# Kernel tuning notes

Hardware: AMD Instinct MI355X
Metric: run time of the kernel (lower is better)

Reference implementation:

```python
import jax, jax.numpy as jnp
import numpy as np

B, T, D, H = 32, 1024, 768, 768

def setup_inputs() -> dict:
    key = jax.random.key(0)
    k0, k1, k2, k3 = jax.random.split(key, 4)
    inputs = jax.random.normal(k0, (B, T, D), dtype=jnp.float32)
    # packed-sequence lengths: sorted descending, in [1, T]
    lengths = jnp.sort(jax.random.randint(k1, (B,), 1, T + 1))[::-1]
    # parameters (orthogonal-block init approximated by scaled gaussian)
    W_in = jax.random.normal(k2, (6 * H, D), dtype=jnp.float32) / np.sqrt(D)
    b_in = jnp.zeros((6 * H,), dtype=jnp.float32)
    W_s = jax.random.normal(k3, (5 * H, H), dtype=jnp.float32) / np.sqrt(H)
    # state bias: forget-gate block initialized to 1.0, rest 0
    b_s = jnp.zeros((5 * H,), dtype=jnp.float32).at[H:2 * H].set(1.0)
    return {"inputs": inputs, "W_in": W_in, "b_in": b_in,
            "W_s": W_s, "b_s": b_s, "lengths": lengths}

def reference(inputs, W_in, b_in, W_s, b_s, lengths):
    Bb, Tt, Dd = inputs.shape
    Hh = W_s.shape[1]
    # precompute all input projections in one big GEMM: [B,T,6H]
    proj_in = jnp.einsum('btd,kd->btk', inputs, W_in) + b_in
    mask = jnp.arange(Tt)[None, :] < lengths[:, None]  # [B,T] valid timesteps

    def step(carry, xs):
        h, c = carry                    # [B,H] each
        pi, m = xs                      # pi: [B,6H], m: [B] bool
        ps = h @ W_s.T + b_s            # [B,5H] recurrent GEMM
        i = jax.nn.sigmoid(pi[:, 0*Hh:1*Hh] + ps[:, 0*Hh:1*Hh])
        f = jax.nn.sigmoid(pi[:, 1*Hh:2*Hh] + ps[:, 1*Hh:2*Hh])
        g = jnp.tanh(pi[:, 2*Hh:3*Hh] + ps[:, 2*Hh:3*Hh])
        o = jax.nn.sigmoid(pi[:, 3*Hh:4*Hh] + ps[:, 3*Hh:4*Hh])
        c_new = i * g + f * c
        out = o * jnp.tanh(c_new)
        # highway mix
        hw = jax.nn.sigmoid(pi[:, 4*Hh:5*Hh] + ps[:, 4*Hh:5*Hh])
        out = hw * out + (1.0 - hw) * pi[:, 5*Hh:6*Hh]
        mcol = m[:, None]
        h_next = jnp.where(mcol, out, h)      # freeze state past seq length
        c_next = jnp.where(mcol, c_new, c)
        y = jnp.where(mcol, out, 0.0)          # zero outputs past length
        return (h_next, c_next), y

    h0 = jnp.zeros((Bb, Hh), dtype=inputs.dtype)
    c0 = jnp.zeros((Bb, Hh), dtype=inputs.dtype)
    pi_t = jnp.swapaxes(proj_in, 0, 1)  # [T,B,6H]
    m_t = jnp.swapaxes(mask, 0, 1)      # [T,B]
    (h_fin, c_fin), ys = jax.lax.scan(step, (h0, c0), (pi_t, m_t))
    return jnp.swapaxes(ys, 0, 1)       # [B,T,H]
```

## Files before the change

### kernel.cpp

```cpp
#include <hip/hip_runtime.h>
#include <hip/hip_bf16.h>

#define Bb 32
#define Tt 1024
#define Dd 768
#define Hh 768
#define NGRP 2
#define BPG 96
#define GB  16
#define CPB 8
#define NTHREADS 192

#define NWELE ((size_t)6 * Hh * Dd)
#define NSELE ((size_t)5 * Hh * Hh)
#define WS_FLAGS 4096
#define WS_HB    8192
#define HBSZ     (GB * Hh * 2)
#define WS_WGT   (WS_HB + 4 * HBSZ)
#define WS_NEED  (WS_WGT + (NWELE + NSELE) * 2)

typedef short short8 __attribute__((ext_vector_type(8)));
typedef float f4 __attribute__((ext_vector_type(4)));

__device__ __forceinline__ float bf2f(ushort u) {
    unsigned x = (unsigned)u << 16;
    return __builtin_bit_cast(float, x);
}
__device__ __forceinline__ ushort f2bf(float f) {
    unsigned u = __builtin_bit_cast(unsigned, f);
    return (ushort)((u + 0x7fffu + ((u >> 16) & 1u)) >> 16);
}
__device__ __forceinline__ float sigm(float x) { return 1.0f / (1.0f + __expf(-x)); }
__device__ __forceinline__ float tanh_(float x) {
    float e = __expf(2.0f * x);
    return 1.0f - 2.0f / (e + 1.0f);
}

__global__ void prep_nb(const int* __restrict__ len, int* __restrict__ nbArr) {
    int t = blockIdx.x * 256 + threadIdx.x;
    if (t < Tt) {
        int c = 0;
#pragma unroll
        for (int b = 0; b < Bb; ++b) c += (len[b] > t) ? 1 : 0;
        nbArr[t] = c;
    }
}

__global__ void conv_w(const void* __restrict__ Win, const void* __restrict__ Ws,
                       const void* __restrict__ bs, ushort* __restrict__ wOut) {
    const bool isbf = (((const unsigned*)bs)[384] != 0u);
    size_t i = ((size_t)blockIdx.x * 256 + threadIdx.x) * 8;
    if (i >= NWELE + NSELE) return;
    const void* src = (i < NWELE) ? Win : Ws;
    size_t off = (i < NWELE) ? i : (i - NWELE);
    if (isbf) {
        *(uint4*)(wOut + i) = *(const uint4*)((const ushort*)src + off);
    } else {
        const f4* s = (const f4*)((const float*)src + off);
        f4 a = s[0], c = s[1];
        uint4 v;
        v.x = (unsigned)f2bf(a[0]) | ((unsigned)f2bf(a[1]) << 16);
        v.y = (unsigned)f2bf(a[2]) | ((unsigned)f2bf(a[3]) << 16);
        v.z = (unsigned)f2bf(c[0]) | ((unsigned)f2bf(c[1]) << 16);
        v.w = (unsigned)f2bf(c[2]) | ((unsigned)f2bf(c[3]) << 16);
        *(uint4*)(wOut + i) = v;
    }
}

__global__ __launch_bounds__(NTHREADS, 1) void lstm_main(
    const void* __restrict__ inp, const void* __restrict__ bin,
    const void* __restrict__ bs, const int* __restrict__ len,
    void* __restrict__ y, const int* __restrict__ nbArr,
    unsigned* flags, ushort* hbAll, const ushort* __restrict__ wbf)
{
    __shared__ ushort wsL[48 * 776];
    __shared__ ushort hA[GB * 776];
    __shared__ float accT[3][16][16];

    const bool isbf = (((const unsigned*)bs)[384] != 0u);

    const int tid  = threadIdx.x;
    const int lane = tid & 63;
    const int wave = tid >> 6;
    const int g    = blockIdx.x & 1;
    const int w    = blockIdx.x >> 1;
    const int n0   = w * CPB;

    for (int i = tid; i < 48 * 776 / 8; i += NTHREADS)
        *(uint4*)&wsL[i * 8] = uint4{0u, 0u, 0u, 0u};
    const ushort* wbfS = wbf + NWELE;
    __syncthreads();
    for (int i = tid; i < 40 * 96; i += NTHREADS) {
        int c = i / 96, ch = i - c * 96;
        *(uint4*)&wsL[c * 776 + ch * 8] =
            *(const uint4*)(wbfS + ((size_t)((c >> 3) * Hh + n0 + (c & 7))) * Hh + ch * 8);
    }

    float B0 = 0, B1 = 0, B2 = 0, B3 = 0, B4 = 0, B5 = 0, cReg = 0.0f;
    int lenb = 0;
    if (tid < 128) {
        int j = tid & 7, n = n0 + j;
        if (isbf) {
            const ushort* bi = (const ushort*)bin; const ushort* bsp = (const ushort*)bs;
            B0 = bf2f(bi[0 * Hh + n]) + bf2f(bsp[0 * Hh + n]);
            B1 = bf2f(bi[1 * Hh + n]) + bf2f(bsp[1 * Hh + n]);
            B2 = bf2f(bi[2 * Hh + n]) + bf2f(bsp[2 * Hh + n]);
            B3 = bf2f(bi[3 * Hh + n]) + bf2f(bsp[3 * Hh + n]);
            B4 = bf2f(bi[4 * Hh + n]) + bf2f(bsp[4 * Hh + n]);
            B5 = bf2f(bi[5 * Hh + n]);
        } else {
            const float* bi = (const float*)bin; const float* bsp = (const float*)bs;
            B0 = bi[0 * Hh + n] + bsp[0 * Hh + n];
            B1 = bi[1 * Hh + n] + bsp[1 * Hh + n];
            B2 = bi[2 * Hh + n] + bsp[2 * Hh + n];
            B3 = bi[3 * Hh + n] + bsp[3 * Hh + n];
            B4 = bi[4 * Hh + n] + bsp[4 * Hh + n];
            B5 = bi[5 * Hh + n];
        }
        lenb = len[g * GB + (tid >> 3)];
    }

    const int kq = (lane >> 4) << 3;
    const ushort* aP = &hA[(lane & 15) * 776 + kq];
    const int aoff = ((lane >> 4) * 32) + ((lane & 15) * 2);
    const int cc = wave * 16 + (lane & 15);
    const uint4* bPx = (const uint4*)(wbf + ((size_t)((cc >> 3) * Hh + n0 + (cc & 7))) * Dd + kq);
    const ushort* wsP = &wsL[cc * 776 + kq];

    unsigned* flg = flags + g * 128;
    ushort* hb[2] = {hbAll + (g * 2 + 0) * (HBSZ / 2),
                     hbAll + (g * 2 + 1) * (HBSZ / 2)};
    int p = 0;
    long gmax = (1L << 22);
    __syncthreads();

    int tDone = Tt;
    for (int t = 0; t < Tt; ++t) {
        int nbg = nbArr[t] - g * GB;
        nbg = nbg < 0 ? 0 : (nbg > GB ? GB : nbg);
        if (nbg == 0) { tDone = t; break; }

        if (isbf) {
            const ushort* xi = (const ushort*)inp;
            for (int i = tid; i < GB * 96; i += NTHREADS) {
                int row = i / 96, c8 = i - row * 96;
                *(uint4*)&hA[row * 776 + c8 * 8] =
                    *((const uint4*)(xi + ((size_t)(g * GB + row) * Tt + t) * Dd) + c8);
            }
        } else {
            const float* xf = (const float*)inp;
            for (int i = tid; i < GB * 96; i += NTHREADS) {
                int row = i / 96, c8 = i - row * 96;
                const f4* s = (const f4*)(xf + ((size_t)(g * GB + row) * Tt + t) * Dd + c8 * 8);
                f4 a = s[0], c = s[1];
                uint4 v;
                v.x = (unsigned)f2bf(a[0]) | ((unsigned)f2bf(a[1]) << 16);
                v.y = (unsigned)f2bf(a[2]) | ((unsigned)f2bf(a[3]) << 16);
                v.z = (unsigned)f2bf(c[0]) | ((unsigned)f2bf(c[1]) << 16);
                v.w = (unsigned)f2bf(c[2]) | ((unsigned)f2bf(c[3]) << 16);
                *(uint4*)&hA[row * 776 + c8 * 8] = v;
            }
        }
        __syncthreads();

        f4 acc0 = {0, 0, 0, 0}, acc1 = {0, 0, 0, 0};
#pragma unroll
        for (int kb = 0; kb < 24; ++kb) {
            short8 a = __builtin_bit_cast(short8, *(const uint4*)(aP + kb * 32));
            short8 b = __builtin_bit_cast(short8, bPx[kb * 4]);
            if (kb & 1) acc1 = __builtin_amdgcn_mfma_f32_16x16x32_bf16(a, b, acc1, 0, 0, 0);
            else        acc0 = __builtin_amdgcn_mfma_f32_16x16x32_bf16(a, b, acc0, 0, 0, 0);
        }

        if (t > 0) {
            const unsigned target = (unsigned)t;
            long guard = 0;
            for (;;) {
                unsigned f0 = __hip_atomic_load(flg + lane, __ATOMIC_RELAXED,
                                                __HIP_MEMORY_SCOPE_AGENT);
                unsigned f1 = __hip_atomic_load(flg + 32 + lane, __ATOMIC_RELAXED,
                                                __HIP_MEMORY_SCOPE_AGENT);
                bool ok = (f0 >= target) && (f1 >= target);
                if (__all(ok)) break;
                if (++guard > gmax) break;
                __builtin_amdgcn_s_sleep(1);
            }
        }
        __asm__ volatile("" ::: "memory");

        {
            const unsigned long long* aB = (const unsigned long long*)hb[p];
#pragma unroll
            for (int kb = 0; kb < 24; ++kb) {
                unsigned long long v0 = __hip_atomic_load(aB + kb * 128 + aoff,
                                                          __ATOMIC_RELAXED,
                                                          __HIP_MEMORY_SCOPE_AGENT);
                unsigned long long v1 = __hip_atomic_load(aB + kb * 128 + aoff + 1,
                                                          __ATOMIC_RELAXED,
                                                          __HIP_MEMORY_SCOPE_AGENT);
                short8 a;
                __builtin_memcpy(&a, &v0, 8);
                __builtin_memcpy((char*)&a + 8, &v1, 8);
                short8 b = __builtin_bit_cast(short8, *(const uint4*)(wsP + kb * 32));
                if (kb & 1) acc1 = __builtin_amdgcn_mfma_f32_16x16x32_bf16(a, b, acc1, 0, 0, 0);
                else        acc0 = __builtin_amdgcn_mfma_f32_16x16x32_bf16(a, b, acc0, 0, 0, 0);
            }
        }
        {
            f4 s = acc0 + acc1;
            int r0 = (lane >> 4) * 4, col = lane & 15;
#pragma unroll
            for (int i = 0; i < 4; ++i) accT[wave][r0 + i][col] = s[i];
        }
        __syncthreads();

        float outv = 0.0f; bool act = false;
        if (tid < 128) {
            int b = tid >> 3, j = tid & 7;
            float v0 = accT[(0 * 8 + j) >> 4][b][(0 * 8 + j) & 15];
            float v1 = accT[(1 * 8 + j) >> 4][b][(1 * 8 + j) & 15];
            float v2 = accT[(2 * 8 + j) >> 4][b][(2 * 8 + j) & 15];
            float v3 = accT[(3 * 8 + j) >> 4][b][(3 * 8 + j) & 15];
            float v4 = accT[(4 * 8 + j) >> 4][b][(4 * 8 + j) & 15];
            float v5 = accT[(5 * 8 + j) >> 4][b][(5 * 8 + j) & 15];
            float ii = sigm(v0 + B0);
            float ff = sigm(v1 + B1);
            float gg = tanh_(v2 + B2);
            float oo = sigm(v3 + B3);
            float hw = sigm(v4 + B4);
            float p5 = v5 + B5;
            float cn = ii * gg + ff * cReg;
            outv = oo * tanh_(cn);
            outv = hw * outv + (1.0f - hw) * p5;
            act = t < lenb;
            if (act) cReg = cn;

            unsigned myv = (unsigned)f2bf(outv);
            int lane6 = tid & 63;
            int g0 = lane6 & ~3;
            unsigned a0 = (unsigned)__shfl((int)myv, g0 + 0);
            unsigned a1 = (unsigned)__shfl((int)myv, g0 + 1);
            unsigned a2 = (unsigned)__shfl((int)myv, g0 + 2);
            unsigned a3 = (unsigned)__shfl((int)myv, g0 + 3);
            if ((lane6 & 3) == 0 && act) {
                unsigned long long vv = (unsigned long long)(a0 & 0xffffu)
                    | ((unsigned long long)(a1 & 0xffffu) << 16)
                    | ((unsigned long long)(a2 & 0xffffu) << 32)
                    | ((unsigned long long)(a3 & 0xffffu) << 48);
                __hip_atomic_store(
                    (unsigned long long*)(hb[p ^ 1] + w * 128 + b * 8 + j),
                    vv, __ATOMIC_RELAXED, __HIP_MEMORY_SCOPE_AGENT);
            }
        }
        __syncthreads();
        if (tid == 0)
            __hip_atomic_store(flg + w, (unsigned)(t + 1),
                               __ATOMIC_RELAXED, __HIP_MEMORY_SCOPE_AGENT);

        if (tid < 128) {
            int b = tid >> 3, j = tid & 7;
            size_t oi = ((size_t)(g * GB + b) * Tt + t) * Hh + n0 + j;
            if (isbf) ((ushort*)y)[oi] = act ? f2bf(outv) : (ushort)0;
            else      ((float*)y)[oi]  = act ? outv : 0.0f;
        }
        p ^= 1;
    }

    if (tid < 128) {
        int b = tid >> 3, j = tid & 7;
        for (int t = tDone; t < Tt; ++t) {
            size_t oi = ((size_t)(g * GB + b) * Tt + t) * Hh + n0 + j;
            if (isbf) ((ushort*)y)[oi] = 0; else ((float*)y)[oi] = 0.0f;
        }
    }
}

extern "C" void kernel_launch(void* const* d_in, const int* in_sizes, int n_in,
                              void* d_out, int out_size, void* d_ws, size_t ws_size,
                              hipStream_t stream) {
    const void* inp = d_in[0];
    const void* Win = d_in[1];
    const void* bin = d_in[2];
    const void* Ws  = d_in[3];
    const void* bs  = d_in[4];
    const int*  len = (const int*)d_in[5];

    if (ws_size < WS_NEED) return;

    char* ws = (char*)d_ws;
    int* nbArr      = (int*)ws;
    unsigned* flags = (unsigned*)(ws + WS_FLAGS);
    ushort* hbAll   = (ushort*)(ws + WS_HB);
    ushort* wbf     = (ushort*)(ws + WS_WGT);

    hipMemsetAsync(d_ws, 0, WS_WGT, stream);
    prep_nb<<<4, 256, 0, stream>>>(len, nbArr);
    conv_w<<<3168, 256, 0, stream>>>(Win, Ws, bs, wbf);
    lstm_main<<<NGRP * BPG, NTHREADS, 0, stream>>>(inp, bin, bs, len, d_out,
                                                   nbArr, flags, hbAll, wbf);
}
```

Before: 9.403 ms.

## Prefetch next-step inputs, use per-step counters, and batch output stores

The next timestep's input row is prefetched into registers and double-buffered in LDS, so the global load overlaps the current step's GEMM and wait. The per-block flag array polled by all lanes is replaced with one atomic counter per timestep that each wave increments after its h stores. Outputs are staged in LDS and written in groups of 16 timesteps, and four MFMA accumulators replace two. Costs are more registers for the prefetch, more LDS, and a grid-wide counter that every wave hits with an atomic add.

```diff
diff --git a/kernel.cpp b/kernel.cpp
--- a/kernel.cpp
+++ b/kernel.cpp
@@ -10,13 +10,15 @@
 #define GB  16
 #define CPB 8
 #define NTHREADS 192
+#define CNT_TGT (2 * BPG)
 
 #define NWELE ((size_t)6 * Hh * Dd)
 #define NSELE ((size_t)5 * Hh * Hh)
-#define WS_FLAGS 4096
-#define WS_HB    8192
+#define WS_NB    4096
+#define WS_FLG   8192
+#define WS_HBOFF (WS_NB + WS_FLG)
 #define HBSZ     (GB * Hh * 2)
-#define WS_WGT   (WS_HB + 4 * HBSZ)
+#define WS_WGT   (WS_HBOFF + 4 * HBSZ)
 #define WS_NEED  (WS_WGT + (NWELE + NSELE) * 2)
 
 typedef short short8 __attribute__((ext_vector_type(8)));
@@ -74,8 +76,9 @@
     unsigned* flags, ushort* hbAll, const ushort* __restrict__ wbf)
 {
     __shared__ ushort wsL[48 * 776];
-    __shared__ ushort hA[GB * 776];
+    __shared__ ushort hA[2][16 * 776];
     __shared__ float accT[3][16][16];
+    __shared__ float yBuf[16][128];
 
     const bool isbf = (((const unsigned*)bs)[384] != 0u);
 
@@ -121,17 +124,39 @@
     }
 
     const int kq = (lane >> 4) << 3;
-    const ushort* aP = &hA[(lane & 15) * 776 + kq];
+    const int aOff = (lane & 15) * 776 + kq;
     const int aoff = ((lane >> 4) * 32) + ((lane & 15) * 2);
     const int cc = wave * 16 + (lane & 15);
     const uint4* bPx = (const uint4*)(wbf + ((size_t)((cc >> 3) * Hh + n0 + (cc & 7))) * Dd + kq);
     const ushort* wsP = &wsL[cc * 776 + kq];
 
-    unsigned* flg = flags + g * 128;
+    unsigned* cnt = flags + g * Tt;
     ushort* hb[2] = {hbAll + (g * 2 + 0) * (HBSZ / 2),
                      hbAll + (g * 2 + 1) * (HBSZ / 2)};
     int p = 0;
     long gmax = (1L << 22);
+
+    if (isbf) {
+        const ushort* xi = (const ushort*)inp;
+        for (int i = tid; i < GB * 96; i += NTHREADS) {
+            int row = i / 96, c8 = i - row * 96;
+            *(uint4*)&hA[0][row * 776 + c8 * 8] =
+                *((const uint4*)(xi + ((size_t)(g * GB + row) * Tt) * Dd) + c8);
+        }
+    } else {
+        const float* xf = (const float*)inp;
+        for (int i = tid; i < GB * 96; i += NTHREADS) {
+            int row = i / 96, c8 = i - row * 96;
+            const f4* s = (const f4*)(xf + ((size_t)(g * GB + row) * Tt) * Dd + c8 * 8);
+            f4 a = s[0], c = s[1];
+            uint4 v;
+            v.x = (unsigned)f2bf(a[0]) | ((unsigned)f2bf(a[1]) << 16);
+            v.y = (unsigned)f2bf(a[2]) | ((unsigned)f2bf(a[3]) << 16);
+            v.z = (unsigned)f2bf(c[0]) | ((unsigned)f2bf(c[1]) << 16);
+            v.w = (unsigned)f2bf(c[2]) | ((unsigned)f2bf(c[3]) << 16);
+            *(uint4*)&hA[0][row * 776 + c8 * 8] = v;
+        }
+    }
     __syncthreads();
 
     int tDone = Tt;
@@ -140,48 +165,48 @@
         nbg = nbg < 0 ? 0 : (nbg > GB ? GB : nbg);
         if (nbg == 0) { tDone = t; break; }
 
-        if (isbf) {
-            const ushort* xi = (const ushort*)inp;
-            for (int i = tid; i < GB * 96; i += NTHREADS) {
-                int row = i / 96, c8 = i - row * 96;
-                *(uint4*)&hA[row * 776 + c8 * 8] =
-                    *((const uint4*)(xi + ((size_t)(g * GB + row) * Tt + t) * Dd) + c8);
-            }
-        } else {
-            const float* xf = (const float*)inp;
-            for (int i = tid; i < GB * 96; i += NTHREADS) {
-                int row = i / 96, c8 = i - row * 96;
-                const f4* s = (const f4*)(xf + ((size_t)(g * GB + row) * Tt + t) * Dd + c8 * 8);
-                f4 a = s[0], c = s[1];
-                uint4 v;
-                v.x = (unsigned)f2bf(a[0]) | ((unsigned)f2bf(a[1]) << 16);
-                v.y = (unsigned)f2bf(a[2]) | ((unsigned)f2bf(a[3]) << 16);
-                v.z = (unsigned)f2bf(c[0]) | ((unsigned)f2bf(c[1]) << 16);
-                v.w = (unsigned)f2bf(c[2]) | ((unsigned)f2bf(c[3]) << 16);
-                *(uint4*)&hA[row * 776 + c8 * 8] = v;
-            }
-        }
-        __syncthreads();
-
+        uint4 pfA[8], pfB[8];
+        const bool havePf = (t + 1 < Tt);
+        if (havePf) {
+            if (isbf) {
+                const ushort* xi = (const ushort*)inp;
+#pragma unroll
+                for (int ii = 0; ii < 8; ++ii) {
+                    int i = tid + ii * NTHREADS;
+                    int row = i / 96, c8 = i - row * 96;
+                    pfA[ii] = *((const uint4*)(xi + ((size_t)(g * GB + row) * Tt + (t + 1)) * Dd) + c8);
+                }
+            } else {
+                const float* xf = (const float*)inp;
+#pragma unroll
+                for (int ii = 0; ii < 8; ++ii) {
+                    int i = tid + ii * NTHREADS;
+                    int row = i / 96, c8 = i - row * 96;
+                    const uint4* s = (const uint4*)(xf + ((size_t)(g * GB + row) * Tt + (t + 1)) * Dd + c8 * 8);
+                    pfA[ii] = s[0]; pfB[ii] = s[1];
+                }
+            }
+        }
+
+        const ushort* aP = &hA[t & 1][0] + aOff;
         f4 acc0 = {0, 0, 0, 0}, acc1 = {0, 0, 0, 0};
+        f4 acc2 = {0, 0, 0, 0}, acc3 = {0, 0, 0, 0};
 #pragma unroll
         for (int kb = 0; kb < 24; ++kb) {
             short8 a = __builtin_bit_cast(short8, *(const uint4*)(aP + kb * 32));
             short8 b = __builtin_bit_cast(short8, bPx[kb * 4]);
-            if (kb & 1) acc1 = __builtin_amdgcn_mfma_f32_16x16x32_bf16(a, b, acc1, 0, 0, 0);
-            else        acc0 = __builtin_amdgcn_mfma_f32_16x16x32_bf16(a, b, acc0, 0, 0, 0);
+            switch (kb & 3) {
+            case 0: acc0 = __builtin_amdgcn_mfma_f32_16x16x32_bf16(a, b, acc0, 0, 0, 0); break;
+            case 1: acc1 = __builtin_amdgcn_mfma_f32_16x16x32_bf16(a, b, acc1, 0, 0, 0); break;
+            case 2: acc2 = __builtin_amdgcn_mfma_f32_16x16x32_bf16(a, b, acc2, 0, 0, 0); break;
+            default: acc3 = __builtin_amdgcn_mfma_f32_16x16x32_bf16(a, b, acc3, 0, 0, 0); break;
+            }
         }
 
         if (t > 0) {
-            const unsigned target = (unsigned)t;
             long guard = 0;
-            for (;;) {
-                unsigned f0 = __hip_atomic_load(flg + lane, __ATOMIC_RELAXED,
-                                                __HIP_MEMORY_SCOPE_AGENT);
-                unsigned f1 = __hip_atomic_load(flg + 32 + lane, __ATOMIC_RELAXED,
-                                                __HIP_MEMORY_SCOPE_AGENT);
-                bool ok = (f0 >= target) && (f1 >= target);
-                if (__all(ok)) break;
+            while (__hip_atomic_load(cnt + (t - 1), __ATOMIC_RELAXED,
+                                     __HIP_MEMORY_SCOPE_AGENT) < (unsigned)CNT_TGT) {
                 if (++guard > gmax) break;
                 __builtin_amdgcn_s_sleep(1);
             }
@@ -202,19 +227,54 @@
                 __builtin_memcpy(&a, &v0, 8);
                 __builtin_memcpy((char*)&a + 8, &v1, 8);
                 short8 b = __builtin_bit_cast(short8, *(const uint4*)(wsP + kb * 32));
-                if (kb & 1) acc1 = __builtin_amdgcn_mfma_f32_16x16x32_bf16(a, b, acc1, 0, 0, 0);
-                else        acc0 = __builtin_amdgcn_mfma_f32_16x16x32_bf16(a, b, acc0, 0, 0, 0);
+                switch (kb & 3) {
+                case 0: acc0 = __builtin_amdgcn_mfma_f32_16x16x32_bf16(a, b, acc0, 0, 0, 0); break;
+                case 1: acc1 = __builtin_amdgcn_mfma_f32_16x16x32_bf16(a, b, acc1, 0, 0, 0); break;
+                case 2: acc2 = __builtin_amdgcn_mfma_f32_16x16x32_bf16(a, b, acc2, 0, 0, 0); break;
+                default: acc3 = __builtin_amdgcn_mfma_f32_16x16x32_bf16(a, b, acc3, 0, 0, 0); break;
+                }
             }
         }
         {
-            f4 s = acc0 + acc1;
+            f4 s = (acc0 + acc1) + (acc2 + acc3);
             int r0 = (lane >> 4) * 4, col = lane & 15;
 #pragma unroll
             for (int i = 0; i < 4; ++i) accT[wave][r0 + i][col] = s[i];
         }
         __syncthreads();
 
-        float outv = 0.0f; bool act = false;
+        if (havePf) {
+            ushort* hN = &hA[(t + 1) & 1][0];
+            if (isbf) {
+#pragma unroll
+                for (int ii = 0; ii < 8; ++ii) {
+                    int i = tid + ii * NTHREADS;
+                    int row = i / 96, c8 = i - row * 96;
+                    *(uint4*)&hN[row * 776 + c8 * 8] = pfA[ii];
+                }
+            } else {
+#pragma unroll
+                for (int ii = 0; ii < 8; ++ii) {
+                    int i = tid + ii * NTHREADS;
+                    int row = i / 96, c8 = i - row * 96;
+                    float f0 = __builtin_bit_cast(float, pfA[ii].x);
+                    float f1 = __builtin_bit_cast(float, pfA[ii].y);
+                    float f2 = __builtin_bit_cast(float, pfA[ii].z);
+                    float f3 = __builtin_bit_cast(float, pfA[ii].w);
+                    float f4_ = __builtin_bit_cast(float, pfB[ii].x);
+                    float f5 = __builtin_bit_cast(float, pfB[ii].y);
+                    float f6 = __builtin_bit_cast(float, pfB[ii].z);
+                    float f7 = __builtin_bit_cast(float, pfB[ii].w);
+                    uint4 v;
+                    v.x = (unsigned)f2bf(f0) | ((unsigned)f2bf(f1) << 16);
+                    v.y = (unsigned)f2bf(f2) | ((unsigned)f2bf(f3) << 16);
+                    v.z = (unsigned)f2bf(f4_) | ((unsigned)f2bf(f5) << 16);
+                    v.w = (unsigned)f2bf(f6) | ((unsigned)f2bf(f7) << 16);
+                    *(uint4*)&hN[row * 776 + c8 * 8] = v;
+                }
+            }
+        }
+
         if (tid < 128) {
             int b = tid >> 3, j = tid & 7;
             float v0 = accT[(0 * 8 + j) >> 4][b][(0 * 8 + j) & 15];
@@ -230,10 +290,11 @@
             float hw = sigm(v4 + B4);
             float p5 = v5 + B5;
             float cn = ii * gg + ff * cReg;
-            outv = oo * tanh_(cn);
+            float outv = oo * tanh_(cn);
             outv = hw * outv + (1.0f - hw) * p5;
-            act = t < lenb;
+            bool act = t < lenb;
             if (act) cReg = cn;
+            yBuf[t & 15][tid] = act ? outv : 0.0f;
 
             unsigned myv = (unsigned)f2bf(outv);
             int lane6 = tid & 63;
@@ -251,23 +312,36 @@
                     (unsigned long long*)(hb[p ^ 1] + w * 128 + b * 8 + j),
                     vv, __ATOMIC_RELAXED, __HIP_MEMORY_SCOPE_AGENT);
             }
+            __asm__ volatile("s_waitcnt vmcnt(0)" ::: "memory");
+            if ((tid & 63) == 0)
+                __hip_atomic_fetch_add(cnt + t, 1u, __ATOMIC_RELAXED,
+                                       __HIP_MEMORY_SCOPE_AGENT);
         }
         __syncthreads();
-        if (tid == 0)
-            __hip_atomic_store(flg + w, (unsigned)(t + 1),
-                               __ATOMIC_RELAXED, __HIP_MEMORY_SCOPE_AGENT);
-
-        if (tid < 128) {
+
+        if ((t & 15) == 15 && tid < 128) {
             int b = tid >> 3, j = tid & 7;
-            size_t oi = ((size_t)(g * GB + b) * Tt + t) * Hh + n0 + j;
-            if (isbf) ((ushort*)y)[oi] = act ? f2bf(outv) : (ushort)0;
-            else      ((float*)y)[oi]  = act ? outv : 0.0f;
+            int tBase = t - 15;
+#pragma unroll
+            for (int r = 0; r < 16; ++r) {
+                size_t oi = ((size_t)(g * GB + b) * Tt + (tBase + r)) * Hh + n0 + j;
+                float yv = yBuf[r][tid];
+                if (isbf) ((ushort*)y)[oi] = f2bf(yv);
+                else      ((float*)y)[oi]  = yv;
+            }
         }
         p ^= 1;
     }
 
     if (tid < 128) {
         int b = tid >> 3, j = tid & 7;
+        int tBase = tDone & ~15;
+        for (int r = 0; r < (tDone & 15); ++r) {
+            size_t oi = ((size_t)(g * GB + b) * Tt + (tBase + r)) * Hh + n0 + j;
+            float yv = yBuf[r][tid];
+            if (isbf) ((ushort*)y)[oi] = f2bf(yv);
+            else      ((float*)y)[oi]  = yv;
+        }
         for (int t = tDone; t < Tt; ++t) {
             size_t oi = ((size_t)(g * GB + b) * Tt + t) * Hh + n0 + j;
             if (isbf) ((ushort*)y)[oi] = 0; else ((float*)y)[oi] = 0.0f;
@@ -289,8 +363,8 @@
 
     char* ws = (char*)d_ws;
     int* nbArr      = (int*)ws;
-    unsigned* flags = (unsigned*)(ws + WS_FLAGS);
-    ushort* hbAll   = (ushort*)(ws + WS_HB);
+    unsigned* flags = (unsigned*)(ws + WS_NB);
+    ushort* hbAll   = (ushort*)(ws + WS_HBOFF);
     ushort* wbf     = (ushort*)(ws + WS_WGT);
 
     hipMemsetAsync(d_ws, 0, WS_WGT, stream);
```

Result: slower. 11.23 ms (+19.4%).

## Use per-wave flags with replicated copies and single-wave polling for step sync

Applied to the files above, without the earlier changes.

Each of the two elementwise waves now publishes its own step flag right after its h stores drain, which removes the block-wide barrier before flag publication. Flags are written to two replicas, and odd and even blocks poll different replicas to spread the load. Only wave 0 spins on the global flags and then signals the other waves through a shared-memory variable. The MFMA accumulation is also split across four accumulators instead of two to lengthen the dependency chains, at the cost of more polling loads and extra flag stores.

```diff
diff --git a/kernel.cpp b/kernel.cpp
--- a/kernel.cpp
+++ b/kernel.cpp
@@ -13,10 +13,11 @@
 
 #define NWELE ((size_t)6 * Hh * Dd)
 #define NSELE ((size_t)5 * Hh * Hh)
-#define WS_FLAGS 4096
-#define WS_HB    8192
+#define WS_NB    4096
+#define WS_FLG   8192
+#define WS_HBOFF (WS_NB + WS_FLG)
 #define HBSZ     (GB * Hh * 2)
-#define WS_WGT   (WS_HB + 4 * HBSZ)
+#define WS_WGT   (WS_HBOFF + 4 * HBSZ)
 #define WS_NEED  (WS_WGT + (NWELE + NSELE) * 2)
 
 typedef short short8 __attribute__((ext_vector_type(8)));
@@ -76,6 +77,7 @@
     __shared__ ushort wsL[48 * 776];
     __shared__ ushort hA[GB * 776];
     __shared__ float accT[3][16][16];
+    __shared__ int step_rdy;
 
     const bool isbf = (((const unsigned*)bs)[384] != 0u);
 
@@ -85,6 +87,8 @@
     const int g    = blockIdx.x & 1;
     const int w    = blockIdx.x >> 1;
     const int n0   = w * CPB;
+
+    if (tid == 0) step_rdy = 0;
 
     for (int i = tid; i < 48 * 776 / 8; i += NTHREADS)
         *(uint4*)&wsL[i * 8] = uint4{0u, 0u, 0u, 0u};
@@ -127,7 +131,8 @@
     const uint4* bPx = (const uint4*)(wbf + ((size_t)((cc >> 3) * Hh + n0 + (cc & 7))) * Dd + kq);
     const ushort* wsP = &wsL[cc * 776 + kq];
 
-    unsigned* flg = flags + g * 128;
+    unsigned* wflg = flags + g * 512;
+    const int repo = (w & 1) ? 256 : 0;
     ushort* hb[2] = {hbAll + (g * 2 + 0) * (HBSZ / 2),
                      hbAll + (g * 2 + 1) * (HBSZ / 2)};
     int p = 0;
@@ -164,26 +169,45 @@
         __syncthreads();
 
         f4 acc0 = {0, 0, 0, 0}, acc1 = {0, 0, 0, 0};
+        f4 acc2 = {0, 0, 0, 0}, acc3 = {0, 0, 0, 0};
 #pragma unroll
         for (int kb = 0; kb < 24; ++kb) {
             short8 a = __builtin_bit_cast(short8, *(const uint4*)(aP + kb * 32));
             short8 b = __builtin_bit_cast(short8, bPx[kb * 4]);
-            if (kb & 1) acc1 = __builtin_amdgcn_mfma_f32_16x16x32_bf16(a, b, acc1, 0, 0, 0);
-            else        acc0 = __builtin_amdgcn_mfma_f32_16x16x32_bf16(a, b, acc0, 0, 0, 0);
+            switch (kb & 3) {
+            case 0: acc0 = __builtin_amdgcn_mfma_f32_16x16x32_bf16(a, b, acc0, 0, 0, 0); break;
+            case 1: acc1 = __builtin_amdgcn_mfma_f32_16x16x32_bf16(a, b, acc1, 0, 0, 0); break;
+            case 2: acc2 = __builtin_amdgcn_mfma_f32_16x16x32_bf16(a, b, acc2, 0, 0, 0); break;
+            default: acc3 = __builtin_amdgcn_mfma_f32_16x16x32_bf16(a, b, acc3, 0, 0, 0); break;
+            }
         }
 
         if (t > 0) {
-            const unsigned target = (unsigned)t;
-            long guard = 0;
-            for (;;) {
-                unsigned f0 = __hip_atomic_load(flg + lane, __ATOMIC_RELAXED,
-                                                __HIP_MEMORY_SCOPE_AGENT);
-                unsigned f1 = __hip_atomic_load(flg + 32 + lane, __ATOMIC_RELAXED,
-                                                __HIP_MEMORY_SCOPE_AGENT);
-                bool ok = (f0 >= target) && (f1 >= target);
-                if (__all(ok)) break;
-                if (++guard > gmax) break;
-                __builtin_amdgcn_s_sleep(1);
+            if (wave == 0) {
+                const unsigned target = (unsigned)t;
+                long guard = 0;
+                for (;;) {
+                    unsigned f0 = __hip_atomic_load(wflg + repo + lane,
+                                                    __ATOMIC_RELAXED, __HIP_MEMORY_SCOPE_AGENT);
+                    unsigned f1 = __hip_atomic_load(wflg + repo + 64 + lane,
+                                                    __ATOMIC_RELAXED, __HIP_MEMORY_SCOPE_AGENT);
+                    unsigned f2 = __hip_atomic_load(wflg + repo + 128 + lane,
+                                                    __ATOMIC_RELAXED, __HIP_MEMORY_SCOPE_AGENT);
+                    bool ok = (f0 >= target) && (f1 >= target) && (f2 >= target);
+                    if (__all(ok)) break;
+                    if (++guard > gmax) break;
+                    __builtin_amdgcn_s_sleep(2);
+                }
+                if (lane == 0)
+                    __hip_atomic_store(&step_rdy, t, __ATOMIC_RELAXED,
+                                       __HIP_MEMORY_SCOPE_WORKGROUP);
+            } else {
+                long guard = 0;
+                while (__hip_atomic_load(&step_rdy, __ATOMIC_RELAXED,
+                                         __HIP_MEMORY_SCOPE_WORKGROUP) < t) {
+                    if (++guard > gmax) break;
+                    __builtin_amdgcn_s_sleep(1);
+                }
             }
         }
         __asm__ volatile("" ::: "memory");
@@ -202,19 +226,22 @@
                 __builtin_memcpy(&a, &v0, 8);
                 __builtin_memcpy((char*)&a + 8, &v1, 8);
                 short8 b = __builtin_bit_cast(short8, *(const uint4*)(wsP + kb * 32));
-                if (kb & 1) acc1 = __builtin_amdgcn_mfma_f32_16x16x32_bf16(a, b, acc1, 0, 0, 0);
-                else        acc0 = __builtin_amdgcn_mfma_f32_16x16x32_bf16(a, b, acc0, 0, 0, 0);
+                switch (kb & 3) {
+                case 0: acc0 = __builtin_amdgcn_mfma_f32_16x16x32_bf16(a, b, acc0, 0, 0, 0); break;
+                case 1: acc1 = __builtin_amdgcn_mfma_f32_16x16x32_bf16(a, b, acc1, 0, 0, 0); break;
+                case 2: acc2 = __builtin_amdgcn_mfma_f32_16x16x32_bf16(a, b, acc2, 0, 0, 0); break;
+                default: acc3 = __builtin_amdgcn_mfma_f32_16x16x32_bf16(a, b, acc3, 0, 0, 0); break;
+                }
             }
         }
         {
-            f4 s = acc0 + acc1;
+            f4 s = (acc0 + acc1) + (acc2 + acc3);
             int r0 = (lane >> 4) * 4, col = lane & 15;
 #pragma unroll
             for (int i = 0; i < 4; ++i) accT[wave][r0 + i][col] = s[i];
         }
         __syncthreads();
 
-        float outv = 0.0f; bool act = false;
         if (tid < 128) {
             int b = tid >> 3, j = tid & 7;
             float v0 = accT[(0 * 8 + j) >> 4][b][(0 * 8 + j) & 15];
@@ -230,9 +257,9 @@
             float hw = sigm(v4 + B4);
             float p5 = v5 + B5;
             float cn = ii * gg + ff * cReg;
-            outv = oo * tanh_(cn);
+            float outv = oo * tanh_(cn);
             outv = hw * outv + (1.0f - hw) * p5;
-            act = t < lenb;
+            bool act = t < lenb;
             if (act) cReg = cn;
 
             unsigned myv = (unsigned)f2bf(outv);
@@ -251,14 +278,15 @@
                     (unsigned long long*)(hb[p ^ 1] + w * 128 + b * 8 + j),
                     vv, __ATOMIC_RELAXED, __HIP_MEMORY_SCOPE_AGENT);
             }
-        }
-        __syncthreads();
-        if (tid == 0)
-            __hip_atomic_store(flg + w, (unsigned)(t + 1),
-                               __ATOMIC_RELAXED, __HIP_MEMORY_SCOPE_AGENT);
-
-        if (tid < 128) {
-            int b = tid >> 3, j = tid & 7;
+            __asm__ volatile("s_waitcnt vmcnt(0)" ::: "memory");
+            if (lane6 == 0) {
+                int idx = w * 2 + (tid >> 6);
+                __hip_atomic_store(wflg + idx, (unsigned)(t + 1),
+                                   __ATOMIC_RELAXED, __HIP_MEMORY_SCOPE_AGENT);
+                __hip_atomic_store(wflg + 256 + idx, (unsigned)(t + 1),
+                                   __ATOMIC_RELAXED, __HIP_MEMORY_SCOPE_AGENT);
+            }
+
             size_t oi = ((size_t)(g * GB + b) * Tt + t) * Hh + n0 + j;
             if (isbf) ((ushort*)y)[oi] = act ? f2bf(outv) : (ushort)0;
             else      ((float*)y)[oi]  = act ? outv : 0.0f;
@@ -289,8 +317,8 @@
 
     char* ws = (char*)d_ws;
     int* nbArr      = (int*)ws;
-    unsigned* flags = (unsigned*)(ws + WS_FLAGS);
-    ushort* hbAll   = (ushort*)(ws + WS_HB);
+    unsigned* flags = (unsigned*)(ws + WS_NB);
+    ushort* hbAll   = (ushort*)(ws + WS_HBOFF);
     ushort* wbf     = (ushort*)(ws + WS_WGT);
 
     hipMemsetAsync(d_ws, 0, WS_WGT, stream);
```

After: 9.613 ms. +2.2%, slower.
